# Kernel optimization log

Measured on AMD Instinct MI355X. Metric: run time of the kernel, lower is better.

## Reference

```python
import jax, jax.numpy as jnp
import numpy as np

D_MODEL = 256; N_HEADS = 8; N_LEVELS = 4; N_POINTS = 4; D_FF = 2048
SHAPES = [(128, 128), (64, 64), (32, 32), (16, 16)]  # (H_l, W_l) per level
LV = sum(h * w for h, w in SHAPES)  # 21760
B = 8; NQ = 900
EPS = 1e-5


def layer_norm(x, s, b):
    m = x.mean(-1, keepdims=True)
    v = x.var(-1, keepdims=True)
    return (x - m) * jax.lax.rsqrt(v + EPS) * s + b


def mha(q, k, v, in_w, in_b, out_w, out_b):
    # torch nn.MultiheadAttention, batch_first, eval mode (no dropout)
    Bq, Lq, C = q.shape
    h = N_HEADS; d = C // h
    wq, wk, wv = jnp.split(in_w, 3, axis=0)
    bq, bk, bv = jnp.split(in_b, 3)
    qh = (q @ wq.T + bq).reshape(Bq, Lq, h, d)
    kh = (k @ wk.T + bk).reshape(Bq, -1, h, d)
    vh = (v @ wv.T + bv).reshape(Bq, -1, h, d)
    scale = jnp.asarray(1.0 / np.sqrt(d), q.dtype)
    attn = jax.nn.softmax(jnp.einsum('bqhd,bkhd->bhqk', qh, kh) * scale, axis=-1)
    o = jnp.einsum('bhqk,bkhd->bqhd', attn, vh).reshape(Bq, Lq, C)
    return o @ out_w.T + out_b


def deform_attn(query, ref, memory, spatial_shapes, val_w, val_b, off_w, off_b, aw_w, aw_b, co_w, co_b):
    # MSDeformAttn forward (eval): offsets/weights from query, bilinear sample value per level/point
    Bq, Lq, C = query.shape
    h, L, P = N_HEADS, N_LEVELS, N_POINTS
    dh = C // h
    value = (memory @ val_w.T + val_b).reshape(Bq, -1, h, dh)  # (B, Lv, h, dh)
    off = (query @ off_w.T + off_b).reshape(Bq, Lq, h, L, P, 2)
    aw = jax.nn.softmax((query @ aw_w.T + aw_b).reshape(Bq, Lq, h, L * P), axis=-1)
    aw = aw.reshape(Bq, Lq, h, L, P)
    # normalizer = (W_l, H_l) per level
    normalizer = spatial_shapes[:, ::-1].astype(query.dtype)
    loc = ref[:, :, None, :, None, :] + off / normalizer[None, None, None, :, None, :]  # (B,Lq,h,L,P,2)
    out = jnp.zeros((Bq, h, Lq, dh), query.dtype)
    start = 0
    for l, (Hl, Wl) in enumerate(SHAPES):
        v_l = value[:, start:start + Hl * Wl].transpose(0, 2, 1, 3)  # (B,h,Hl*Wl,dh)
        start += Hl * Wl
        xy = loc[:, :, :, l]  # (B,Lq,h,P,2) normalized in [0,1]
        # grid_sample align_corners=False pixel coords
        x = xy[..., 0] * Wl - 0.5
        y = xy[..., 1] * Hl - 0.5
        x0 = jnp.floor(x); y0 = jnp.floor(y)
        wx = x - x0; wy = y - y0
        acc = jnp.zeros((Bq, h, Lq * P, dh), query.dtype)
        for dx, dy, w in ((0, 0, (1 - wx) * (1 - wy)), (1, 0, wx * (1 - wy)),
                          (0, 1, (1 - wx) * wy), (1, 1, wx * wy)):
            xi = x0 + dx; yi = y0 + dy
            valid = (xi >= 0) & (xi <= Wl - 1) & (yi >= 0) & (yi <= Hl - 1)
            xi = jnp.clip(xi, 0, Wl - 1).astype(jnp.int32)
            yi = jnp.clip(yi, 0, Hl - 1).astype(jnp.int32)
            idx = (yi * Wl + xi).transpose(0, 2, 1, 3).reshape(Bq, h, Lq * P)
            g = jnp.take_along_axis(v_l, idx[..., None], axis=2)  # (B,h,Lq*P,dh)
            wgt = (w * valid).transpose(0, 2, 1, 3).reshape(Bq, h, Lq * P)
            acc = acc + g * wgt[..., None]
        acc = acc.reshape(Bq, h, Lq, P, dh)
        wl = aw[:, :, :, l].transpose(0, 2, 1, 3)  # (B,h,Lq,P)
        out = out + jnp.einsum('bhqpd,bhqp->bhqd', acc, wl)
    out = out.transpose(0, 2, 1, 3).reshape(Bq, Lq, C)
    return out @ co_w.T + co_b


def forward(tgt, memory, query_pos, reference_points, sa_in_w, sa_in_b, sa_out_w, sa_out_b,
            off_w, off_b, aw_w, aw_b, val_w, val_b, co_w, co_b,
            l1_w, l1_b, l2_w, l2_b, ln1_s, ln1_b, ln2_s, ln2_b, ln3_s, ln3_b, spatial_shapes):
    q = tgt + query_pos  # with_pos_embed; eval mode: no group_detr split, no dropout
    tgt2 = mha(q, q, tgt, sa_in_w, sa_in_b, sa_out_w, sa_out_b)
    tgt = layer_norm(tgt + tgt2, ln1_s, ln1_b)
    tgt2 = deform_attn(tgt + query_pos, reference_points, memory, spatial_shapes,
                       val_w, val_b, off_w, off_b, aw_w, aw_b, co_w, co_b)
    tgt = layer_norm(tgt + tgt2, ln2_s, ln2_b)
    tgt2 = jax.nn.relu(tgt @ l1_w.T + l1_b) @ l2_w.T + l2_b
    return layer_norm(tgt + tgt2, ln3_s, ln3_b)


def setup_inputs():
    key = jax.random.key(0)
    ks = jax.random.split(key, 16)
    C = D_MODEL
    f = lambda i, shape, s=0.02: jax.random.normal(ks[i], shape, jnp.float32) * s
    HLP = N_HEADS * N_LEVELS * N_POINTS
    return {
        'tgt': f(0, (B, NQ, C), 1.0),
        'memory': f(1, (B, LV, C), 1.0),
        'query_pos': f(2, (B, NQ, C), 1.0),
        'reference_points': jax.random.uniform(ks[3], (B, NQ, N_LEVELS, 2), jnp.float32),
        'sa_in_w': f(4, (3 * C, C)), 'sa_in_b': jnp.zeros((3 * C,), jnp.float32),
        'sa_out_w': f(5, (C, C)), 'sa_out_b': jnp.zeros((C,), jnp.float32),
        'off_w': f(6, (HLP * 2, C)), 'off_b': f(7, (HLP * 2,), 0.5),
        'aw_w': f(8, (HLP, C)), 'aw_b': jnp.zeros((HLP,), jnp.float32),
        'val_w': f(9, (C, C)), 'val_b': jnp.zeros((C,), jnp.float32),
        'co_w': f(10, (C, C)), 'co_b': jnp.zeros((C,), jnp.float32),
        'l1_w': f(11, (D_FF, C)), 'l1_b': jnp.zeros((D_FF,), jnp.float32),
        'l2_w': f(12, (C, D_FF)), 'l2_b': jnp.zeros((C,), jnp.float32),
        'ln1_s': jnp.ones((C,), jnp.float32), 'ln1_b': jnp.zeros((C,), jnp.float32),
        'ln2_s': jnp.ones((C,), jnp.float32), 'ln2_b': jnp.zeros((C,), jnp.float32),
        'ln3_s': jnp.ones((C,), jnp.float32), 'ln3_b': jnp.zeros((C,), jnp.float32),
        'spatial_shapes': jnp.asarray(SHAPES, jnp.int32),
        'level_start_index': jnp.asarray(np.cumsum([0] + [h * w for h, w in SHAPES[:-1]]), jnp.int32),
    }


def reference(tgt, memory, query_pos, reference_points, sa_in_w, sa_in_b, sa_out_w, sa_out_b,
              off_w, off_b, aw_w, aw_b, val_w, val_b, co_w, co_b,
              l1_w, l1_b, l2_w, l2_b, ln1_s, ln1_b, ln2_s, ln2_b, ln3_s, ln3_b,
              spatial_shapes, level_start_index):
    return forward(tgt, memory, query_pos, reference_points, sa_in_w, sa_in_b, sa_out_w, sa_out_b,
                   off_w, off_b, aw_w, aw_b, val_w, val_b, co_w, co_b,
                   l1_w, l1_b, l2_w, l2_b, ln1_s, ln1_b, ln2_s, ln2_b, ln3_s, ln3_b, spatial_shapes)
```

## Files before the change

### kernel.cpp

```cpp
#include <hip/hip_runtime.h>
#include <hip/hip_bf16.h>

#define NQL 900
#define CDIM 256
#define BDIM 8
#define LVTOT 21760

typedef __bf16 bf16x8 __attribute__((ext_vector_type(8)));
typedef float f32x4 __attribute__((ext_vector_type(4)));
typedef uint u32x4 __attribute__((ext_vector_type(4)));
typedef uint u32x2 __attribute__((ext_vector_type(2)));

__device__ __forceinline__ ushort f2bf(float x) {
  uint u = __builtin_bit_cast(uint, x);
  u += 0x7fff + ((u >> 16) & 1);
  return (ushort)(u >> 16);
}

template <bool ABF16, bool AADD, bool RELU, bool OUTBF16>
__global__ __launch_bounds__(256, 4) void mgemm_kernel(const void* __restrict__ Ap,
                                                       const float* __restrict__ A2p,
                                                       const float* __restrict__ W,
                                                       const float* __restrict__ bias,
                                                       void* __restrict__ Cout,
                                                       int M, int N, int K) {
  __shared__ ushort smem[10240];
  ushort* As = smem;
  ushort* Bs = smem + 5120;
  const int tid = threadIdx.x;
  const int m0 = blockIdx.y * 128, n0 = blockIdx.x * 128;
  const int wv = tid >> 6;
  const int wm = (wv >> 1) * 64, wn = (wv & 1) * 64;
  const int lane = tid & 63;
  const int lr = lane & 15, kq = lane >> 4;

  f32x4 acc[4][4] = {};
  float4 pa[2][2], pb[2][2];
  u32x4 pa16[2];

  auto load_tiles = [&](int k0) {
#pragma unroll
    for (int it = 0; it < 2; ++it) {
      int idx = it * 256 + tid;
      int r = idx >> 2, s = (idx & 3) << 3;
      int gm = min(m0 + r, M - 1);
      if constexpr (ABF16) {
        pa16[it] = *(const u32x4*)((const ushort*)Ap + (size_t)gm * K + k0 + s);
      } else {
        const float* ap = (const float*)Ap + (size_t)gm * K + k0 + s;
        pa[it][0] = *(const float4*)ap;
        pa[it][1] = *(const float4*)(ap + 4);
        if constexpr (AADD) {
          const float* ap2 = A2p + (size_t)gm * K + k0 + s;
          float4 q0 = *(const float4*)ap2;
          float4 q1 = *(const float4*)(ap2 + 4);
          pa[it][0].x += q0.x; pa[it][0].y += q0.y; pa[it][0].z += q0.z; pa[it][0].w += q0.w;
          pa[it][1].x += q1.x; pa[it][1].y += q1.y; pa[it][1].z += q1.z; pa[it][1].w += q1.w;
        }
      }
      int gn = min(n0 + r, N - 1);
      const float* wp = W + (size_t)gn * K + k0 + s;
      pb[it][0] = *(const float4*)wp;
      pb[it][1] = *(const float4*)(wp + 4);
    }
  };

  auto store_tiles = [&]() {
#pragma unroll
    for (int it = 0; it < 2; ++it) {
      int idx = it * 256 + tid;
      int r = idx >> 2, s = (idx & 3) << 3;
      u32x4 u;
      if constexpr (ABF16) {
        u = pa16[it];
      } else {
        u.x = f2bf(pa[it][0].x) | ((uint)f2bf(pa[it][0].y) << 16);
        u.y = f2bf(pa[it][0].z) | ((uint)f2bf(pa[it][0].w) << 16);
        u.z = f2bf(pa[it][1].x) | ((uint)f2bf(pa[it][1].y) << 16);
        u.w = f2bf(pa[it][1].z) | ((uint)f2bf(pa[it][1].w) << 16);
      }
      *(u32x4*)&As[r * 40 + s] = u;
      u32x4 w;
      w.x = f2bf(pb[it][0].x) | ((uint)f2bf(pb[it][0].y) << 16);
      w.y = f2bf(pb[it][0].z) | ((uint)f2bf(pb[it][0].w) << 16);
      w.z = f2bf(pb[it][1].x) | ((uint)f2bf(pb[it][1].y) << 16);
      w.w = f2bf(pb[it][1].z) | ((uint)f2bf(pb[it][1].w) << 16);
      *(u32x4*)&Bs[r * 40 + s] = w;
    }
  };

  load_tiles(0);
  for (int k0 = 0; k0 < K; k0 += 32) {
    store_tiles();
    __syncthreads();
    if (k0 + 32 < K) load_tiles(k0 + 32);
    bf16x8 af[4], bq[4];
#pragma unroll
    for (int m = 0; m < 4; ++m)
      af[m] = __builtin_bit_cast(bf16x8, *(const u32x4*)&As[(wm + m * 16 + lr) * 40 + kq * 8]);
#pragma unroll
    for (int n = 0; n < 4; ++n)
      bq[n] = __builtin_bit_cast(bf16x8, *(const u32x4*)&Bs[(wn + n * 16 + lr) * 40 + kq * 8]);
#pragma unroll
    for (int m = 0; m < 4; ++m)
#pragma unroll
      for (int n = 0; n < 4; ++n)
        acc[m][n] = __builtin_amdgcn_mfma_f32_16x16x32_bf16(af[m], bq[n], acc[m][n], 0, 0, 0);
    __syncthreads();
  }

  if constexpr (OUTBF16) {
    ushort* Cs = smem;
#pragma unroll
    for (int p = 0; p < 2; ++p) {
      __syncthreads();
      if (wm == p * 64) {
#pragma unroll
        for (int n = 0; n < 4; ++n) {
          int col = wn + n * 16 + lr;
          float bv = bias[n0 + col];
#pragma unroll
          for (int m = 0; m < 4; ++m)
#pragma unroll
            for (int j = 0; j < 4; ++j) {
              float v = acc[m][n][j] + bv;
              if (RELU) v = fmaxf(v, 0.f);
              Cs[(m * 16 + kq * 4 + j) * 136 + col] = f2bf(v);
            }
        }
      }
      __syncthreads();
#pragma unroll
      for (int it = 0; it < 4; ++it) {
        int idx = it * 256 + tid;
        int r = idx >> 4, c = (idx & 15) * 8;
        int grow = m0 + p * 64 + r;
        if (grow < M) {
          u32x4 u = *(const u32x4*)&Cs[r * 136 + c];
          *(u32x4*)((ushort*)Cout + (size_t)grow * N + n0 + c) = u;
        }
      }
    }
  } else {
#pragma unroll
    for (int n = 0; n < 4; ++n) {
      int gcol = n0 + wn + n * 16 + lr;
      float bv = bias[gcol];
#pragma unroll
      for (int m = 0; m < 4; ++m) {
        int rbase = m0 + wm + m * 16 + kq * 4;
#pragma unroll
        for (int j = 0; j < 4; ++j) {
          int grow = rbase + j;
          if (grow >= M) continue;
          float v = acc[m][n][j] + bv;
          if (RELU) v = fmaxf(v, 0.f);
          ((float*)Cout)[(size_t)grow * N + gcol] = v;
        }
      }
    }
  }
}

template <bool ABF16, bool AADD, bool RELU, bool HASRES, bool DOSM, bool OUTBF16>
__global__ __launch_bounds__(256, 4) void mgemm64_kernel(const void* __restrict__ Ap,
                                                         const float* __restrict__ A2p,
                                                         const float* __restrict__ W,
                                                         const float* __restrict__ bias,
                                                         const float* __restrict__ Rres,
                                                         void* __restrict__ Cout,
                                                         int M, int N, int K) {
  __shared__ ushort smem[5120];
  ushort* As = smem;
  ushort* Bs = smem + 2560;
  const int tid = threadIdx.x;
  const int m0 = blockIdx.y * 64, n0 = blockIdx.x * 64;
  const int wv = tid >> 6, lane = tid & 63;
  const int wm = (wv >> 1) * 32, wn = (wv & 1) * 32;
  const int lr = lane & 15, kq = lane >> 4;

  f32x4 acc[2][2] = {};
  float4 pa[2], pb[2];
  u32x4 pa16;

  auto load_tiles = [&](int k0) {
    int r = tid >> 2, s = (tid & 3) << 3;
    int gm = min(m0 + r, M - 1);
    if constexpr (ABF16) {
      pa16 = *(const u32x4*)((const ushort*)Ap + (size_t)gm * K + k0 + s);
    } else {
      const float* ap = (const float*)Ap + (size_t)gm * K + k0 + s;
      pa[0] = *(const float4*)ap;
      pa[1] = *(const float4*)(ap + 4);
      if constexpr (AADD) {
        const float* ap2 = A2p + (size_t)gm * K + k0 + s;
        float4 q0 = *(const float4*)ap2;
        float4 q1 = *(const float4*)(ap2 + 4);
        pa[0].x += q0.x; pa[0].y += q0.y; pa[0].z += q0.z; pa[0].w += q0.w;
        pa[1].x += q1.x; pa[1].y += q1.y; pa[1].z += q1.z; pa[1].w += q1.w;
      }
    }
    int gn = min(n0 + r, N - 1);
    const float* wp = W + (size_t)gn * K + k0 + s;
    pb[0] = *(const float4*)wp;
    pb[1] = *(const float4*)(wp + 4);
  };

  auto store_tiles = [&]() {
    int r = tid >> 2, s = (tid & 3) << 3;
    u32x4 u;
    if constexpr (ABF16) {
      u = pa16;
    } else {
      u.x = f2bf(pa[0].x) | ((uint)f2bf(pa[0].y) << 16);
      u.y = f2bf(pa[0].z) | ((uint)f2bf(pa[0].w) << 16);
      u.z = f2bf(pa[1].x) | ((uint)f2bf(pa[1].y) << 16);
      u.w = f2bf(pa[1].z) | ((uint)f2bf(pa[1].w) << 16);
    }
    *(u32x4*)&As[r * 40 + s] = u;
    u32x4 w;
    w.x = f2bf(pb[0].x) | ((uint)f2bf(pb[0].y) << 16);
    w.y = f2bf(pb[0].z) | ((uint)f2bf(pb[0].w) << 16);
    w.z = f2bf(pb[1].x) | ((uint)f2bf(pb[1].y) << 16);
    w.w = f2bf(pb[1].z) | ((uint)f2bf(pb[1].w) << 16);
    *(u32x4*)&Bs[r * 40 + s] = w;
  };

  load_tiles(0);
  for (int k0 = 0; k0 < K; k0 += 32) {
    store_tiles();
    __syncthreads();
    if (k0 + 32 < K) load_tiles(k0 + 32);
    bf16x8 af[2], bq[2];
#pragma unroll
    for (int m = 0; m < 2; ++m)
      af[m] = __builtin_bit_cast(bf16x8, *(const u32x4*)&As[(wm + m * 16 + lr) * 40 + kq * 8]);
#pragma unroll
    for (int n = 0; n < 2; ++n)
      bq[n] = __builtin_bit_cast(bf16x8, *(const u32x4*)&Bs[(wn + n * 16 + lr) * 40 + kq * 8]);
#pragma unroll
    for (int m = 0; m < 2; ++m)
#pragma unroll
      for (int n = 0; n < 2; ++n)
        acc[m][n] = __builtin_amdgcn_mfma_f32_16x16x32_bf16(af[m], bq[n], acc[m][n], 0, 0, 0);
    __syncthreads();
  }

  if constexpr (OUTBF16) {
    ushort* Cs = smem;
    __syncthreads();
#pragma unroll
    for (int n = 0; n < 2; ++n) {
      int col = wn + n * 16 + lr;
      float bv = bias[n0 + col];
#pragma unroll
      for (int m = 0; m < 2; ++m)
#pragma unroll
        for (int j = 0; j < 4; ++j) {
          float v = acc[m][n][j] + bv;
          if (RELU) v = fmaxf(v, 0.f);
          Cs[(wm + m * 16 + kq * 4 + j) * 72 + col] = f2bf(v);
        }
    }
    __syncthreads();
#pragma unroll
    for (int it = 0; it < 2; ++it) {
      int idx = it * 256 + tid;
      int r = idx >> 3, c = (idx & 7) * 8;
      int grow = m0 + r;
      if (grow < M) {
        u32x4 u = *(const u32x4*)&Cs[r * 72 + c];
        *(u32x4*)((ushort*)Cout + (size_t)grow * N + n0 + c) = u;
      }
    }
  } else {
#pragma unroll
    for (int n = 0; n < 2; ++n) {
      int gcol = n0 + wn + n * 16 + lr;
      float bv = bias[gcol];
#pragma unroll
      for (int m = 0; m < 2; ++m) {
        int rbase = m0 + wm + m * 16 + kq * 4;
#pragma unroll
        for (int j = 0; j < 4; ++j) {
          int grow = rbase + j;
          float v = acc[m][n][j] + bv;
          if constexpr (DOSM) {
            float gmax = v;
#pragma unroll
            for (int w = 1; w < 16; w <<= 1) gmax = fmaxf(gmax, __shfl_xor(gmax, w));
            float e = __expf(v - gmax);
            float gs = e;
#pragma unroll
            for (int w = 1; w < 16; w <<= 1) gs += __shfl_xor(gs, w);
            v = e / gs;
          }
          if (grow >= M) continue;
          if (HASRES) v += Rres[(size_t)grow * N + gcol];
          if (RELU) v = fmaxf(v, 0.f);
          ((float*)Cout)[(size_t)grow * N + gcol] = v;
        }
      }
    }
  }
}

__global__ __launch_bounds__(256) void wconv_kernel(const float* __restrict__ W,
                                                    ushort* __restrict__ Wbf) {
  int idx = (blockIdx.x * 256 + threadIdx.x) * 4;
  float4 v = *(const float4*)(W + idx);
  u32x2 u;
  u.x = f2bf(v.x) | ((uint)f2bf(v.y) << 16);
  u.y = f2bf(v.z) | ((uint)f2bf(v.w) << 16);
  *(u32x2*)(Wbf + idx) = u;
}

__global__ __launch_bounds__(256, 2) void vproj_kernel(const float* __restrict__ A,
                                                       const ushort* __restrict__ Wbf,
                                                       const float* __restrict__ bias,
                                                       ushort* __restrict__ Cout) {
  __shared__ ushort As[64 * 264];
  __shared__ ushort Bs[256 * 40];
  const int tid = threadIdx.x;
  const int m0 = blockIdx.x * 64;
  const int wv = tid >> 6, lane = tid & 63;
  const int lr = lane & 15, kq = lane >> 4;

  {
    const float* base = A + (size_t)m0 * 256;
    float4 v[16];
#pragma unroll
    for (int it = 0; it < 16; ++it)
      v[it] = *(const float4*)(base + (size_t)(it * 256 + tid) * 4);
#pragma unroll
    for (int it = 0; it < 16; ++it) {
      int f4 = it * 256 + tid;
      int row = f4 >> 6;
      int col = (f4 & 63) * 4;
      u32x2 w;
      w.x = f2bf(v[it].x) | ((uint)f2bf(v[it].y) << 16);
      w.y = f2bf(v[it].z) | ((uint)f2bf(v[it].w) << 16);
      *(u32x2*)&As[row * 264 + col] = w;
    }
  }

  u32x4 pw[4];
  auto loadW = [&](int k0) {
#pragma unroll
    for (int i = 0; i < 4; ++i)
      pw[i] = *(const u32x4*)(Wbf + (size_t)tid * 256 + k0 + i * 8);
  };
  auto storeW = [&]() {
#pragma unroll
    for (int i = 0; i < 4; ++i)
      *(u32x4*)&Bs[tid * 40 + i * 8] = pw[i];
  };

  f32x4 acc[16] = {};
  loadW(0);
  for (int k0 = 0; k0 < 256; k0 += 32) {
    storeW();
    __syncthreads();
    if (k0 + 32 < 256) loadW(k0 + 32);
    bf16x8 af = __builtin_bit_cast(bf16x8,
        *(const u32x4*)&As[(wv * 16 + lr) * 264 + k0 + kq * 8]);
#pragma unroll
    for (int ng = 0; ng < 16; ++ng) {
      bf16x8 bq = __builtin_bit_cast(bf16x8, *(const u32x4*)&Bs[(ng * 16 + lr) * 40 + kq * 8]);
      acc[ng] = __builtin_amdgcn_mfma_f32_16x16x32_bf16(af, bq, acc[ng], 0, 0, 0);
    }
    __syncthreads();
  }

  ushort* Cs = As;
#pragma unroll
  for (int nf = 0; nf < 16; ++nf) {
    int col = nf * 16 + lr;
    float bv = bias[col];
#pragma unroll
    for (int j = 0; j < 4; ++j) {
      int row = wv * 16 + kq * 4 + j;
      Cs[row * 264 + col] = f2bf(acc[nf][j] + bv);
    }
  }
  __syncthreads();
#pragma unroll
  for (int it = 0; it < 8; ++it) {
    int idx = it * 256 + tid;
    int r = idx >> 5, c = (idx & 31) * 8;
    u32x4 u = *(const u32x4*)&Cs[r * 264 + c];
    *(u32x4*)(Cout + (size_t)(m0 + r) * 256 + c) = u;
  }
}

__global__ __launch_bounds__(256) void vt_kernel(const ushort* __restrict__ tmp_v,
                                                 ushort* __restrict__ vt) {
  __shared__ ushort Ls[64 * 40];
  const int qt = blockIdx.x;
  const int bh = blockIdx.y;
  const int b = bh >> 3, h = bh & 7;
  const int tid = threadIdx.x;
  const int q0 = qt * 64;
  {
    int r = tid >> 2, c = (tid & 3) * 8;
    int gq = min(q0 + r, NQL - 1);
    u32x4 u = *(const u32x4*)(tmp_v + ((size_t)(b * NQL + gq) * 256) + h * 32 + c);
    *(u32x4*)&Ls[r * 40 + c] = u;
  }
  __syncthreads();
  {
    int d = tid >> 3, qw = (tid & 7) * 8;
    u32x4 u;
    uint w[8];
#pragma unroll
    for (int j = 0; j < 8; ++j) w[j] = Ls[(qw + j) * 40 + d];
    u.x = w[0] | (w[1] << 16);
    u.y = w[2] | (w[3] << 16);
    u.z = w[4] | (w[5] << 16);
    u.w = w[6] | (w[7] << 16);
    *(u32x4*)(vt + ((size_t)(bh * 32 + d) * 960) + q0 + qw) = u;
  }
}

__global__ __launch_bounds__(256, 2) void fattn_kernel(const ushort* __restrict__ qk,
                                                       const ushort* __restrict__ vt,
                                                       float* __restrict__ out) {
  __shared__ ushort Ks[64 * 40];
  __shared__ ushort Vs[32 * 72];
  __shared__ ushort Ps[4][16 * 72];
  const int qt = blockIdx.x, bh = blockIdx.y;
  const int b = bh >> 3, h = bh & 7;
  const int tid = threadIdx.x;
  const int wv = tid >> 6, lane = tid & 63;
  const int lq = lane & 15, hi = lane >> 4;
  const int q0 = qt * 64 + wv * 16;
  const float SC = 0.17677669529663689f;

  bf16x8 qfrag;
  {
    int qrow = min(q0 + lq, NQL - 1);
    qfrag = __builtin_bit_cast(bf16x8,
        *(const u32x4*)(qk + (size_t)(b * NQL + qrow) * 512 + h * 32 + hi * 8));
  }

  f32x4 o0 = {}, o1 = {};
  float mrow = -1e30f, lrow = 0.f;

  for (int kt = 0; kt < 15; ++kt) {
    const int k0 = kt * 64;
    __syncthreads();
    {
      int r = tid >> 2, c = (tid & 3) * 8;
      int gk = min(k0 + r, NQL - 1);
      u32x4 u = *(const u32x4*)(qk + (size_t)(b * NQL + gk) * 512 + 256 + h * 32 + c);
      *(u32x4*)&Ks[r * 40 + c] = u;
    }
    {
      int r = tid >> 3, c = (tid & 7) * 8;
      u32x4 u = *(const u32x4*)(vt + (size_t)(bh * 32 + r) * 960 + k0 + c);
      *(u32x4*)&Vs[r * 72 + c] = u;
    }
    __syncthreads();

    f32x4 st[4];
#pragma unroll
    for (int mt = 0; mt < 4; ++mt) {
      bf16x8 kf = __builtin_bit_cast(bf16x8, *(const u32x4*)&Ks[(mt * 16 + lq) * 40 + hi * 8]);
      f32x4 z = {};
      st[mt] = __builtin_amdgcn_mfma_f32_16x16x32_bf16(kf, qfrag, z, 0, 0, 0);
    }
    float sv[4][4];
    float lmax = -1e30f;
#pragma unroll
    for (int mt = 0; mt < 4; ++mt)
#pragma unroll
      for (int j = 0; j < 4; ++j) {
        int key = k0 + mt * 16 + hi * 4 + j;
        float v = st[mt][j] * SC;
        v = (key < NQL) ? v : -1e30f;
        sv[mt][j] = v;
        lmax = fmaxf(lmax, v);
      }
    lmax = fmaxf(lmax, __shfl_xor(lmax, 16));
    lmax = fmaxf(lmax, __shfl_xor(lmax, 32));
    float mnew = fmaxf(mrow, lmax);
    float rs = __expf(mrow - mnew);
    float lsum = 0.f;
    uint pw[4][2];
#pragma unroll
    for (int mt = 0; mt < 4; ++mt) {
      float p0 = __expf(sv[mt][0] - mnew);
      float p1 = __expf(sv[mt][1] - mnew);
      float p2 = __expf(sv[mt][2] - mnew);
      float p3 = __expf(sv[mt][3] - mnew);
      lsum += (p0 + p1) + (p2 + p3);
      pw[mt][0] = f2bf(p0) | ((uint)f2bf(p1) << 16);
      pw[mt][1] = f2bf(p2) | ((uint)f2bf(p3) << 16);
    }
    lsum += __shfl_xor(lsum, 16);
    lsum += __shfl_xor(lsum, 32);
    lrow = lrow * rs + lsum;
    mrow = mnew;
#pragma unroll
    for (int j = 0; j < 4; ++j) {
      float rsj = __shfl(rs, hi * 4 + j);
      o0[j] *= rsj;
      o1[j] *= rsj;
    }
#pragma unroll
    for (int mt = 0; mt < 4; ++mt) {
      u32x2 u;
      u.x = pw[mt][0];
      u.y = pw[mt][1];
      *(u32x2*)&Ps[wv][lq * 72 + mt * 16 + hi * 4] = u;
    }
#pragma unroll
    for (int k2 = 0; k2 < 2; ++k2) {
      bf16x8 pa = __builtin_bit_cast(bf16x8, *(const u32x4*)&Ps[wv][lq * 72 + k2 * 32 + hi * 8]);
      bf16x8 vb0 = __builtin_bit_cast(bf16x8, *(const u32x4*)&Vs[(0 * 16 + lq) * 72 + k2 * 32 + hi * 8]);
      bf16x8 vb1 = __builtin_bit_cast(bf16x8, *(const u32x4*)&Vs[(1 * 16 + lq) * 72 + k2 * 32 + hi * 8]);
      o0 = __builtin_amdgcn_mfma_f32_16x16x32_bf16(pa, vb0, o0, 0, 0, 0);
      o1 = __builtin_amdgcn_mfma_f32_16x16x32_bf16(pa, vb1, o1, 0, 0, 0);
    }
  }

#pragma unroll
  for (int j = 0; j < 4; ++j) {
    float lj = __shfl(lrow, hi * 4 + j);
    float inv = 1.f / lj;
    int gq = q0 + hi * 4 + j;
    if (gq < NQL) {
      float* op = out + (size_t)(b * NQL + gq) * 256 + h * 32;
      op[lq] = o0[j] * inv;
      op[16 + lq] = o1[j] * inv;
    }
  }
}

__global__ __launch_bounds__(256) void ln_kernel(const float* __restrict__ x,
                                                 const float* __restrict__ s,
                                                 const float* __restrict__ bb,
                                                 float* __restrict__ out, int M) {
  const int wv = threadIdx.x >> 6, lane = threadIdx.x & 63;
  const int row = blockIdx.x * 4 + wv;
  if (row >= M) return;
  const float4 v = *(const float4*)(x + (size_t)row * 256 + lane * 4);
  float s1 = (v.x + v.y) + (v.z + v.w);
  float s2 = (v.x * v.x + v.y * v.y) + (v.z * v.z + v.w * v.w);
#pragma unroll
  for (int w = 1; w < 64; w <<= 1) {
    s1 += __shfl_xor(s1, w);
    s2 += __shfl_xor(s2, w);
  }
  float mean = s1 * (1.f / 256.f);
  float var = s2 * (1.f / 256.f) - mean * mean;
  float inv = rsqrtf(var + 1e-5f);
  float4 sc = *(const float4*)(s + lane * 4);
  float4 bv = *(const float4*)(bb + lane * 4);
  float4 o;
  o.x = (v.x - mean) * inv * sc.x + bv.x;
  o.y = (v.y - mean) * inv * sc.y + bv.y;
  o.z = (v.z - mean) * inv * sc.z + bv.z;
  o.w = (v.w - mean) * inv * sc.w + bv.w;
  *(float4*)(out + (size_t)row * 256 + lane * 4) = o;
}

__global__ __launch_bounds__(256) void deform_kernel(const __hip_bfloat16* __restrict__ value,
                                                     const float* __restrict__ offb,
                                                     const float* __restrict__ awb,
                                                     const float* __restrict__ refp,
                                                     float* __restrict__ dfout) {
  const int Hs[4] = {128, 64, 32, 16};
  const int Stl[4] = {0, 16384, 20480, 21504};
  int row = blockIdx.x;
  int b = row / NQL;
  int tid = threadIdx.x;
  int h = tid >> 5, d = tid & 31;
  const float* off = offb + (size_t)row * 256;
  const float* aw = awb + (size_t)row * 128;
  const float* ref = refp + (size_t)row * 8;
  const __hip_bfloat16* vb = value + (size_t)b * LVTOT * 256 + h * 32 + d;
  float acc = 0.f;
#pragma unroll
  for (int l = 0; l < 4; ++l) {
    int Wi = Hs[l], Hi = Hs[l];
    float Wl = (float)Wi, Hl = (float)Hi;
    int st = Stl[l];
    float rx = ref[l * 2 + 0], ry = ref[l * 2 + 1];
#pragma unroll
    for (int p = 0; p < 4; ++p) {
      int oi = ((h * 4 + l) * 4 + p) * 2;
      float x = (rx + off[oi] / Wl) * Wl - 0.5f;
      float y = (ry + off[oi + 1] / Hl) * Hl - 0.5f;
      float w = aw[h * 16 + l * 4 + p];
      float x0f = floorf(x), y0f = floorf(y);
      float wx = x - x0f, wy = y - y0f;
      int xi0 = (int)x0f, yi0 = (int)y0f;
      float samp = 0.f;
#pragma unroll
      for (int dy = 0; dy < 2; ++dy) {
#pragma unroll
        for (int dx = 0; dx < 2; ++dx) {
          int xi = xi0 + dx, yi = yi0 + dy;
          float tw = (dx ? wx : 1.f - wx) * (dy ? wy : 1.f - wy);
          bool valid = (xi >= 0) && (xi < Wi) && (yi >= 0) && (yi < Hi);
          int xc = min(max(xi, 0), Wi - 1);
          int yc = min(max(yi, 0), Hi - 1);
          float vv = __bfloat162float(vb[(size_t)(st + yc * Wi + xc) * 256]);
          samp += valid ? tw * vv : 0.f;
        }
      }
      acc = fmaf(w, samp, acc);
    }
  }
  dfout[(size_t)row * 256 + tid] = acc;
}

extern "C" void kernel_launch(void* const* d_in, const int* in_sizes, int n_in,
                              void* d_out, int out_size, void* d_ws, size_t ws_size,
                              hipStream_t stream) {
  const float* tgt = (const float*)d_in[0];
  const float* memory = (const float*)d_in[1];
  const float* qpos = (const float*)d_in[2];
  const float* refp = (const float*)d_in[3];
  const float* sa_in_w = (const float*)d_in[4];
  const float* sa_in_b = (const float*)d_in[5];
  const float* sa_out_w = (const float*)d_in[6];
  const float* sa_out_b = (const float*)d_in[7];
  const float* off_w = (const float*)d_in[8];
  const float* off_b = (const float*)d_in[9];
  const float* aw_w = (const float*)d_in[10];
  const float* aw_b = (const float*)d_in[11];
  const float* val_w = (const float*)d_in[12];
  const float* val_b = (const float*)d_in[13];
  const float* co_w = (const float*)d_in[14];
  const float* co_b = (const float*)d_in[15];
  const float* l1_w = (const float*)d_in[16];
  const float* l1_b = (const float*)d_in[17];
  const float* l2_w = (const float*)d_in[18];
  const float* l2_b = (const float*)d_in[19];
  const float* ln1_s = (const float*)d_in[20];
  const float* ln1_b = (const float*)d_in[21];
  const float* ln2_s = (const float*)d_in[22];
  const float* ln2_b = (const float*)d_in[23];
  const float* ln3_s = (const float*)d_in[24];
  const float* ln3_b = (const float*)d_in[25];

  float* ws = (float*)d_ws;
  const size_t E = (size_t)BDIM * NQL * CDIM;
  ushort* vt = (ushort*)(ws + E);
  float* attn_o = ws + 4 * E;
  ushort* tmp_qk = (ushort*)(ws + 5 * E);
  ushort* tmp_v = (ushort*)(ws + 7 * E);
  float* sa_out = ws + 5 * E;
  float* offb = ws + E;
  float* awb = ws + 2 * E;
  float* dfout = ws + 3 * E;
  float* co_out = ws + 4 * E;
  ushort* hidden = (ushort*)ws;
  float* ffn_o = ws + 4 * E;
  float* tgt1 = ws + 8 * E;
  float* tgt2 = ws + 9 * E;
  ushort* wbf = (ushort*)(ws + 10 * E);
  ushort* valbf = (ushort*)(ws + 11 * E);

  const int M = BDIM * NQL;
  const int MT = (M + 127) / 128;
  const int M64 = (M + 63) / 64;
  const int LNG = (M + 3) / 4;
  dim3 blk(256);

  wconv_kernel<<<64, blk, 0, stream>>>(val_w, wbf);
  mgemm64_kernel<false, true, false, false, false, true><<<dim3(8, M64), blk, 0, stream>>>(
      tgt, qpos, sa_in_w, sa_in_b, nullptr, tmp_qk, M, 512, 256);
  mgemm64_kernel<false, false, false, false, false, true><<<dim3(4, M64), blk, 0, stream>>>(
      tgt, nullptr, sa_in_w + 512 * 256, sa_in_b + 512, nullptr, tmp_v, M, 256, 256);
  vt_kernel<<<dim3(15, 64), blk, 0, stream>>>(tmp_v, vt);
  fattn_kernel<<<dim3(15, 64), blk, 0, stream>>>(tmp_qk, vt, attn_o);
  mgemm64_kernel<false, false, false, true, false, false><<<dim3(4, M64), blk, 0, stream>>>(
      attn_o, nullptr, sa_out_w, sa_out_b, tgt, sa_out, M, 256, 256);
  ln_kernel<<<LNG, blk, 0, stream>>>(sa_out, ln1_s, ln1_b, tgt1, M);
  vproj_kernel<<<(BDIM * LVTOT) / 64, blk, 0, stream>>>(memory, wbf, val_b, valbf);
  mgemm64_kernel<false, true, false, false, false, false><<<dim3(4, M64), blk, 0, stream>>>(
      tgt1, qpos, off_w, off_b, nullptr, offb, M, 256, 256);
  mgemm64_kernel<false, true, false, false, true, false><<<dim3(2, M64), blk, 0, stream>>>(
      tgt1, qpos, aw_w, aw_b, nullptr, awb, M, 128, 256);
  deform_kernel<<<M, blk, 0, stream>>>((const __hip_bfloat16*)valbf, offb, awb, refp, dfout);
  mgemm64_kernel<false, false, false, true, false, false><<<dim3(4, M64), blk, 0, stream>>>(
      dfout, nullptr, co_w, co_b, tgt1, co_out, M, 256, 256);
  ln_kernel<<<LNG, blk, 0, stream>>>(co_out, ln2_s, ln2_b, tgt2, M);
  mgemm_kernel<false, false, true, true><<<dim3(16, MT), blk, 0, stream>>>(
      tgt2, nullptr, l1_w, l1_b, hidden, M, 2048, 256);
  mgemm64_kernel<true, false, false, true, false, false><<<dim3(4, M64), blk, 0, stream>>>(
      hidden, nullptr, l2_w, l2_b, tgt2, ffn_o, M, 256, 2048);
  ln_kernel<<<LNG, blk, 0, stream>>>(ffn_o, ln3_s, ln3_b, (float*)d_out, M);
}
```

Before: 357.3 us.

## Load value-projection weights directly from global into registers, drop LDS staging

The value projection GEMM no longer stages weight tiles through shared memory. Each wave now owns 64 output columns and computes a 4x4 MFMA tile grid, reading bf16 weights straight from global memory (mostly L2-resident) into registers and reusing the A fragments from LDS. This removes the per-k-step LDS writes and barriers and frees shared memory, and launch bounds are raised to allow four blocks per CU. The cost is more global load traffic per wave, with no explicit prefetch to hide its latency.

```diff
diff --git a/kernel.cpp b/kernel.cpp
--- a/kernel.cpp
+++ b/kernel.cpp
@@ -315,12 +315,11 @@
   *(u32x2*)(Wbf + idx) = u;
 }
 
-__global__ __launch_bounds__(256, 2) void vproj_kernel(const float* __restrict__ A,
+__global__ __launch_bounds__(256, 4) void vproj_kernel(const float* __restrict__ A,
                                                        const ushort* __restrict__ Wbf,
                                                        const float* __restrict__ bias,
                                                        ushort* __restrict__ Cout) {
   __shared__ ushort As[64 * 264];
-  __shared__ ushort Bs[256 * 40];
   const int tid = threadIdx.x;
   const int m0 = blockIdx.x * 64;
   const int wv = tid >> 6, lane = tid & 63;
@@ -343,45 +342,39 @@
       *(u32x2*)&As[row * 264 + col] = w;
     }
   }
-
-  u32x4 pw[4];
-  auto loadW = [&](int k0) {
-#pragma unroll
-    for (int i = 0; i < 4; ++i)
-      pw[i] = *(const u32x4*)(Wbf + (size_t)tid * 256 + k0 + i * 8);
-  };
-  auto storeW = [&]() {
-#pragma unroll
-    for (int i = 0; i < 4; ++i)
-      *(u32x4*)&Bs[tid * 40 + i * 8] = pw[i];
-  };
-
-  f32x4 acc[16] = {};
-  loadW(0);
+  __syncthreads();
+
+  const ushort* wbase = Wbf + (size_t)(wv * 64 + lr) * 256 + kq * 8;
+  f32x4 acc[4][4] = {};
+#pragma unroll
   for (int k0 = 0; k0 < 256; k0 += 32) {
-    storeW();
-    __syncthreads();
-    if (k0 + 32 < 256) loadW(k0 + 32);
-    bf16x8 af = __builtin_bit_cast(bf16x8,
-        *(const u32x4*)&As[(wv * 16 + lr) * 264 + k0 + kq * 8]);
-#pragma unroll
-    for (int ng = 0; ng < 16; ++ng) {
-      bf16x8 bq = __builtin_bit_cast(bf16x8, *(const u32x4*)&Bs[(ng * 16 + lr) * 40 + kq * 8]);
-      acc[ng] = __builtin_amdgcn_mfma_f32_16x16x32_bf16(af, bq, acc[ng], 0, 0, 0);
-    }
-    __syncthreads();
-  }
+    u32x4 bw[4];
+#pragma unroll
+    for (int ng = 0; ng < 4; ++ng)
+      bw[ng] = *(const u32x4*)(wbase + ng * 16 * 256 + k0);
+    bf16x8 af[4];
+#pragma unroll
+    for (int m = 0; m < 4; ++m)
+      af[m] = __builtin_bit_cast(bf16x8, *(const u32x4*)&As[(m * 16 + lr) * 264 + k0 + kq * 8]);
+#pragma unroll
+    for (int m = 0; m < 4; ++m)
+#pragma unroll
+      for (int ng = 0; ng < 4; ++ng)
+        acc[m][ng] = __builtin_amdgcn_mfma_f32_16x16x32_bf16(
+            af[m], __builtin_bit_cast(bf16x8, bw[ng]), acc[m][ng], 0, 0, 0);
+  }
+  __syncthreads();
 
   ushort* Cs = As;
 #pragma unroll
-  for (int nf = 0; nf < 16; ++nf) {
-    int col = nf * 16 + lr;
+  for (int ng = 0; ng < 4; ++ng) {
+    int col = wv * 64 + ng * 16 + lr;
     float bv = bias[col];
 #pragma unroll
-    for (int j = 0; j < 4; ++j) {
-      int row = wv * 16 + kq * 4 + j;
-      Cs[row * 264 + col] = f2bf(acc[nf][j] + bv);
-    }
+    for (int m = 0; m < 4; ++m)
+#pragma unroll
+      for (int j = 0; j < 4; ++j)
+        Cs[(m * 16 + kq * 4 + j) * 264 + col] = f2bf(acc[m][ng][j] + bv);
   }
   __syncthreads();
 #pragma unroll
```

After: 341.4 us. 4.4% less time.
